# Optimization experiments

Measured on AMD Instinct MI355X. Metric: run time of the kernel, lower is better.

The kernel has to match this reference:

```python
import jax, jax.numpy as jnp
import numpy as np

BS, LATENT, HID, MAXLEN = 128, 512, 1024, 512

def setup_inputs() -> dict:
    key = jax.random.key(0)
    ks = jax.random.split(key, 12)
    s = 1.0 / np.sqrt(HID)  # pytorch default LSTM init scale
    inp = {}
    inp["decoder_input"] = jax.random.normal(ks[0], (BS, LATENT), jnp.float32)
    inp["lengths"] = jax.random.randint(ks[1], (BS,), 0, MAXLEN)
    # bidirectional single-layer LSTM params (gate order i,f,g,o; combined bias = b_ih+b_hh)
    inp["Wih_f"] = jax.random.uniform(ks[2], (4 * HID, LATENT), jnp.float32, -s, s)
    inp["Whh_f"] = jax.random.uniform(ks[3], (4 * HID, HID), jnp.float32, -s, s)
    inp["b_f"] = jax.random.uniform(ks[4], (4 * HID,), jnp.float32, -s, s)
    inp["Wih_b"] = jax.random.uniform(ks[5], (4 * HID, LATENT), jnp.float32, -s, s)
    inp["Whh_b"] = jax.random.uniform(ks[6], (4 * HID, HID), jnp.float32, -s, s)
    inp["b_b"] = jax.random.uniform(ks[7], (4 * HID,), jnp.float32, -s, s)
    # out: Linear(hidden -> latent); fc1: Linear(2*hidden -> 1)
    inp["W_out"] = jax.random.uniform(ks[8], (LATENT, HID), jnp.float32, -s, s)
    inp["b_out"] = jax.random.uniform(ks[9], (LATENT,), jnp.float32, -s, s)
    inp["W_fc1"] = jax.random.uniform(ks[10], (1, 2 * HID), jnp.float32, -s, s)
    inp["b_fc1"] = jax.random.uniform(ks[11], (1,), jnp.float32, -s, s)
    return inp

def _lstm_cell(x, h, c, Wih, Whh, b):
    z = x @ Wih.T + h @ Whh.T + b  # (bs, 4H)
    i, f, g, o = jnp.split(z, 4, axis=-1)
    c2 = jax.nn.sigmoid(f) * c + jax.nn.sigmoid(i) * jnp.tanh(g)
    h2 = jax.nn.sigmoid(o) * jnp.tanh(c2)
    return h2, c2

def reference(decoder_input, lengths, Wih_f, Whh_f, b_f, Wih_b, Whh_b, b_b,
              W_out, b_out, W_fc1, b_fc1):
    max_len = int(jnp.max(lengths))  # static decode length
    bs = decoder_input.shape[0]
    h0 = jnp.zeros((bs, HID), decoder_input.dtype)

    def step(carry, _):
        x, hf, cf, hb, cb = carry
        # bidirectional LSTM over a length-1 sequence = two cells on same input
        hf, cf = _lstm_cell(x, hf, cf, Wih_f, Whh_f, b_f)
        hb, cb = _lstm_cell(x, hb, cb, Wih_b, Whh_b, b_b)
        out_t = jnp.concatenate([hf, hb], axis=-1)  # (bs, 2H)
        # next input = out(h_n[-1]) i.e. backward-direction hidden
        x_next = hb @ W_out.T + b_out
        return (x_next, hf, cf, hb, cb), out_t

    carry0 = (decoder_input, h0, h0, h0, h0)
    _, outs = jax.lax.scan(step, carry0, xs=None, length=max_len)  # (T, bs, 2H)
    x = jnp.transpose(outs, (1, 0, 2))  # (bs, T, 2H)
    x = jax.nn.relu(x)
    return x @ W_fc1.T + b_fc1  # (bs, T, 1)
```

## Files before the change

kernel.cpp:

```cpp
#include <hip/hip_runtime.h>
#include <math.h>

typedef unsigned short u16;
typedef __attribute__((ext_vector_type(8))) short short8;
typedef __attribute__((ext_vector_type(4))) float f32x4;

__device__ __forceinline__ float sigm(float x) { return 1.0f / (1.0f + expf(-x)); }

__device__ __forceinline__ u16 f2bf(float x) {
    union { float f; unsigned u; } v; v.f = x;
    unsigned r = v.u + 0x7fffu + ((v.u >> 16) & 1u);
    return (u16)(r >> 16);
}
__device__ __forceinline__ float bf2f(u16 h) {
    union { unsigned u; float f; } v; v.u = ((unsigned)h) << 16;
    return v.f;
}
__device__ __forceinline__ f32x4 mfma16(short8 a, short8 b, f32x4 c) {
    return __builtin_amdgcn_mfma_f32_16x16x32_bf16(a, b, c, 0, 0, 0);
}
__device__ __forceinline__ void gl_lds16(const void* g, void* l) {
    __builtin_amdgcn_global_load_lds(
        (const __attribute__((address_space(1))) unsigned int*)g,
        (__attribute__((address_space(3))) unsigned int*)l, 16, 0, 0);
}
__device__ __forceinline__ int swz(int c) { return (c ^ (c >> 2)) & 3; }

#define FENCE() asm volatile("" ::: "memory")

#define STAGE_W(kk, buf)                                                      \
    do {                                                                      \
        gl_lds16(Wsrc + sA + (kk), sm + (buf) * 8192 + lds0);                 \
        gl_lds16(Wsrc + sB + (kk), sm + (buf) * 8192 + lds1);                 \
    } while (0)

#define LOAD_A(kk, AH_, AL_)                                                  \
    do {                                                                      \
        _Pragma("unroll") for (int ks_ = 0; ks_ < 2; ++ks_) {                 \
            AH_[ks_] = *(const short8*)(Ah + aoff + (kk) + ks_ * 32);         \
            AL_[ks_] = *(const short8*)(Al + aoff + (kk) + ks_ * 32);         \
        }                                                                     \
    } while (0)

#define COMPUTE(bix, AH_, AL_, cix)                                           \
    do {                                                                      \
        const char* bb_ = sm + (bix) * 8192;                                  \
        _Pragma("unroll") for (int ks_ = 0; ks_ < 2; ++ks_) {                 \
            short8 bh_[2], bl_[2];                                            \
            _Pragma("unroll") for (int nt_ = 0; nt_ < 2; ++nt_) {             \
                const int col_ = nt_ * 16 + l15;                              \
                const int off_ = ks_ * 2048 + col_ * 64 + ((quad ^ swz(col_)) * 16); \
                bh_[nt_] = *(const short8*)(bb_ + off_);                      \
                bl_[nt_] = *(const short8*)(bb_ + 4096 + off_);               \
            }                                                                 \
            _Pragma("unroll") for (int nt_ = 0; nt_ < 2; ++nt_) {             \
                acc[nt_] = mfma16(AH_[ks_], bh_[nt_], acc[nt_]);              \
                acc[nt_] = mfma16(AL_[ks_], bh_[nt_], acc[nt_]);              \
                acc[nt_] = mfma16(AH_[ks_], bl_[nt_], acc[nt_]);              \
            }                                                                 \
        }                                                                     \
        if (fc1w) {                                                           \
            const int kb_ = (cix) * 64 + quad * 8;                            \
            _Pragma("unroll") for (int ks_ = 0; ks_ < 2; ++ks_) {             \
                const float* wp_ = smWf + kb_ + ks_ * 32;                     \
                const f32x4 w0_ = *(const f32x4*)(wp_);                       \
                const f32x4 w1_ = *(const f32x4*)(wp_ + 4);                   \
                const short8 hv_ = AH_[ks_];                                  \
                const short8 lv_ = AL_[ks_];                                  \
                _Pragma("unroll") for (int e_ = 0; e_ < 8; ++e_) {            \
                    const float v_ = bf2f((u16)hv_[e_]) + bf2f((u16)lv_[e_]); \
                    const float wv_ = (e_ < 4) ? w0_[e_] : w1_[e_ - 4];       \
                    fsum = fmaf(fmaxf(v_, 0.0f), wv_, fsum);                  \
                }                                                             \
            }                                                                 \
        }                                                                     \
    } while (0)

#define ITER(cc, BC, BS, AHU, ALU, AHL, ALL)                                  \
    do {                                                                      \
        asm volatile("s_waitcnt vmcnt(16)" ::: "memory");                     \
        __builtin_amdgcn_s_barrier();                                         \
        FENCE();                                                              \
        STAGE_W(((cc) + 3) * 64, BS);                                         \
        FENCE();                                                              \
        LOAD_A(((cc) + 3) * 64, AHL, ALL);                                    \
        COMPUTE(BC, AHU, ALU, (cc));                                          \
    } while (0)

__global__ __launch_bounds__(256, 2) void k_step(
    const u16* __restrict__ Ah, const u16* __restrict__ Al,
    u16* __restrict__ NAh, u16* __restrict__ NAl,
    const u16* __restrict__ WH, const u16* __restrict__ WL, int wstride,
    int koff_f, int nch_f, int koff_b, int nch_b,
    const float* __restrict__ BR, float* __restrict__ CF, float* __restrict__ CB,
    const float* __restrict__ Wfc1, const float* __restrict__ bfc1,
    float* __restrict__ out, int T, int t)
{
    __shared__ __align__(16) char sm[32768];
    __shared__ __align__(16) char ze[9216];
    __shared__ __align__(16) float smWf[2048];

    const int tid = threadIdx.x, bid = blockIdx.x;
    const int w = tid >> 6, lane = tid & 63, l15 = lane & 15, quad = lane >> 4;
    const int dir = bid & 1;
    const int rest = bid >> 1;
    const int rowhalf = rest >> 7, colgrp = rest & 127;
    const int nbase = dir * 4096 + colgrp * 32;
    const int koff = dir ? koff_b : koff_f;
    const int nch  = dir ? nch_b : nch_f;
    const int r0 = rowhalf * 64 + w * 16;

    const bool fc1b = (dir == 0) && (colgrp == 0);
    const bool fc1w = fc1b && (t > 0);

    const int sp = w >> 1, skh = w & 1;
    const u16* Wsrc = sp ? WL : WH;
    size_t sA, sB;
    int lds0, lds1;
    {
        const int colA = 0 * 16 + (lane >> 2);
        const int colB = 1 * 16 + (lane >> 2);
        const int sa = (lane & 3) ^ swz(colA);
        const int sb = (lane & 3) ^ swz(colB);
        sA = (size_t)(nbase + colA) * wstride + (size_t)(koff + skh * 32 + sa * 8);
        sB = (size_t)(nbase + colB) * wstride + (size_t)(koff + skh * 32 + sb * 8);
        lds0 = sp * 4096 + skh * 2048;
        lds1 = lds0 + 1024;
    }

    const size_t aoff = (size_t)(r0 + l15) * 2048 + (size_t)(koff + quad * 8);

    f32x4 acc[2] = {};
    short8 ah0[2], al0[2], ah1[2], al1[2];
    short8 ah2[2], al2[2], ah3[2], al3[2];
    float fsum = 0.0f;

    if (fc1b) {
        const f32x4 w0 = *(const f32x4*)(Wfc1 + tid * 8);
        const f32x4 w1 = *(const f32x4*)(Wfc1 + tid * 8 + 4);
        *(f32x4*)(smWf + tid * 8) = w0;
        *(f32x4*)(smWf + tid * 8 + 4) = w1;
    }
    asm volatile("s_waitcnt lgkmcnt(0)" ::: "memory");

    STAGE_W(0, 0);   FENCE(); LOAD_A(0, ah0, al0);   FENCE();
    STAGE_W(64, 1);  FENCE(); LOAD_A(64, ah1, al1);  FENCE();
    STAGE_W(128, 2); FENCE(); LOAD_A(128, ah2, al2); FENCE();

    for (int c = 0; c < nch; c += 4) {
        ITER(c + 0, 0, 3, ah0, al0, ah3, al3);
        ITER(c + 1, 1, 0, ah1, al1, ah0, al0);
        ITER(c + 2, 2, 1, ah2, al2, ah1, al1);
        ITER(c + 3, 3, 2, ah3, al3, ah2, al2);
    }
    asm volatile("s_waitcnt vmcnt(0)" ::: "memory");

    if (fc1w) {
        float v = fsum;
        v += __shfl_xor(v, 16);
        v += __shfl_xor(v, 32);
        if (lane < 16)
            out[(size_t)(r0 + l15) * T + (t - 1)] = v + bfc1[0];
    }

    char* zb = ze + w * 2304;
#pragma unroll
    for (int nt = 0; nt < 2; ++nt)
#pragma unroll
        for (int r = 0; r < 4; ++r)
            *(float*)(zb + (quad * 4 + r) * 144 + (nt * 16 + l15) * 4) = acc[nt][r];

    float* C = dir ? CB : CF;
    const int ul = lane & 7;
#pragma unroll
    for (int p2 = 0; p2 < 2; ++p2) {
        const int ml = p2 * 8 + (lane >> 3);
        const f32x4 z = *(const f32x4*)(zb + ml * 144 + ul * 16);
        const f32x4 b4 = *(const f32x4*)(BR + nbase + ul * 4);
        const float zi = z[0] + b4[0], zf = z[1] + b4[1];
        const float zg = z[2] + b4[2], zo = z[3] + b4[3];
        const int u = colgrp * 8 + ul;
        const int m = r0 + ml;
        const size_t cidx = (size_t)m * 1024 + u;
        const float cold = C[cidx];
        const float c2 = sigm(zf) * cold + sigm(zi) * tanhf(zg);
        const float h2 = sigm(zo) * tanhf(c2);
        C[cidx] = c2;
        const size_t hidx = (size_t)m * 2048 + dir * 1024 + u;
        const u16 hh = f2bf(h2);
        NAh[hidx] = hh;
        NAl[hidx] = f2bf(h2 - bf2f(hh));
    }
}

__global__ __launch_bounds__(256) void k_tail(
    const u16* __restrict__ Ah, const u16* __restrict__ Al,
    const float* __restrict__ Wfc1, const float* __restrict__ bfc1,
    float* __restrict__ out, int T)
{
    __shared__ float red[256];
    const int m = blockIdx.x, tid = threadIdx.x;
    const size_t base = (size_t)m * 2048 + tid * 8;
    const short8 hv = *(const short8*)(Ah + base);
    const short8 lv = *(const short8*)(Al + base);
    float s = 0.0f;
#pragma unroll
    for (int e = 0; e < 8; ++e) {
        const float v = bf2f((u16)hv[e]) + bf2f((u16)lv[e]);
        s = fmaf(fmaxf(v, 0.0f), Wfc1[tid * 8 + e], s);
    }
    red[tid] = s;
    __syncthreads();
    for (int off = 128; off > 0; off >>= 1) {
        if (tid < off) red[tid] += red[tid + off];
        __syncthreads();
    }
    if (tid == 0) out[(size_t)m * T + T - 1] = red[0] + bfc1[0];
}

__global__ __launch_bounds__(256, 1) void k_fold(
    const u16* __restrict__ AH, const u16* __restrict__ AL,
    const u16* __restrict__ BH, const u16* __restrict__ BL,
    const float* __restrict__ Whh_b,
    u16* __restrict__ WH, u16* __restrict__ WL)
{
    const int tid = threadIdx.x, bid = blockIdx.x;
    const int w = tid >> 6, lane = tid & 63, l15 = lane & 15, quad = lane >> 4;
    const int bm = bid >> 4, bn = bid & 15;
    const int ar0 = bm * 64 + (w & 1) * 32;
    const int br0 = bn * 64 + (w >> 1) * 32;
    f32x4 acc[2][2] = {};
    for (int k0 = 0; k0 < 512; k0 += 32) {
        short8 a_h[2], a_l[2], b_h[2], b_l[2];
#pragma unroll
        for (int mt = 0; mt < 2; ++mt) {
            const size_t o = (size_t)(ar0 + mt * 16 + l15) * 512 + k0 + quad * 8;
            a_h[mt] = *(const short8*)(AH + o);
            a_l[mt] = *(const short8*)(AL + o);
        }
#pragma unroll
        for (int nt = 0; nt < 2; ++nt) {
            const size_t o = (size_t)(br0 + nt * 16 + l15) * 512 + k0 + quad * 8;
            b_h[nt] = *(const short8*)(BH + o);
            b_l[nt] = *(const short8*)(BL + o);
        }
#pragma unroll
        for (int mt = 0; mt < 2; ++mt)
#pragma unroll
            for (int nt = 0; nt < 2; ++nt) {
                acc[mt][nt] = mfma16(a_h[mt], b_h[nt], acc[mt][nt]);
                acc[mt][nt] = mfma16(a_l[mt], b_h[nt], acc[mt][nt]);
                acc[mt][nt] = mfma16(a_h[mt], b_l[nt], acc[mt][nt]);
            }
    }
#pragma unroll
    for (int mt = 0; mt < 2; ++mt)
#pragma unroll
        for (int nt = 0; nt < 2; ++nt)
#pragma unroll
            for (int r = 0; r < 4; ++r) {
                const int row = ar0 + mt * 16 + quad * 4 + r;
                const int j = br0 + nt * 16 + l15;
                float v = acc[mt][nt][r];
                if (row >= 4096)
                    v += Whh_b[(size_t)((row & 3) * 1024 + ((row & 4095) >> 2)) * 1024 + j];
                const size_t d = (size_t)row * 2048 + 1024 + j;
                const u16 hh = f2bf(v);
                WH[d] = hh;
                WL[d] = f2bf(v - bf2f(hh));
            }
}

__global__ __launch_bounds__(256) void k_prep(
    const float* __restrict__ dec,
    const float* __restrict__ Wih_f, const float* __restrict__ Whh_f,
    const float* __restrict__ b_f, const float* __restrict__ Wih_b,
    const float* __restrict__ b_b, const float* __restrict__ W_out,
    const float* __restrict__ b_out, const float* __restrict__ b_fc1,
    u16* __restrict__ WihH, u16* __restrict__ WihL,
    u16* __restrict__ WoTH, u16* __restrict__ WoTL,
    float* __restrict__ BR0, float* __restrict__ BR1,
    u16* __restrict__ A0h, u16* __restrict__ A0l,
    u16* __restrict__ WH, u16* __restrict__ WL,
    float* __restrict__ out, int out_size)
{
    const int t = blockIdx.x * 256 + threadIdx.x;
    if (t < 524288) {
        const int colp = t >> 6, kb = (t & 63) * 8;
        const int dir = colp >> 12, u = (colp & 4095) >> 2, g = colp & 3;
        const float* src = (dir ? Wih_b : Wih_f) + (size_t)(g * 1024 + u) * 512 + kb;
        const size_t d = (size_t)colp * 512 + kb;
#pragma unroll
        for (int j = 0; j < 8; ++j) {
            const float v = src[j];
            const u16 hh = f2bf(v);
            WihH[d + j] = hh; WihL[d + j] = f2bf(v - bf2f(hh));
        }
    } else if (t < 589824) {
        const int i = t - 524288, jc = i >> 6, lb = (i & 63) * 8;
#pragma unroll
        for (int jj = 0; jj < 8; ++jj) {
            const float v = W_out[(size_t)(lb + jj) * 1024 + jc];
            const size_t d = (size_t)jc * 512 + lb + jj;
            const u16 hh = f2bf(v);
            WoTH[d] = hh; WoTL[d] = f2bf(v - bf2f(hh));
        }
    } else if (t < 598016) {
        const int colp = t - 589824;
        const int dir = colp >> 12, u = (colp & 4095) >> 2, g = colp & 3;
        const float* Wih = dir ? Wih_b : Wih_f;
        const float s = (dir ? b_b : b_f)[g * 1024 + u];
        BR0[colp] = s;
        float dot = 0.0f;
        for (int l = 0; l < 512; ++l)
            dot += Wih[(size_t)(g * 1024 + u) * 512 + l] * b_out[l];
        BR1[colp] = s + dot;
    } else if (t < 606208) {
        const int i = t - 598016, m = i >> 6, kb = (i & 63) * 8;
#pragma unroll
        for (int j = 0; j < 8; ++j) {
            const float v = dec[(size_t)m * 512 + kb + j];
            const size_t d = (size_t)m * 2048 + kb + j;
            const u16 hh = f2bf(v);
            A0h[d] = hh; A0l[d] = f2bf(v - bf2f(hh));
        }
    } else if (t < 614400) {
        const int base = (t - 606208) * 8;
        const float b0 = b_fc1[0];
#pragma unroll
        for (int j = 0; j < 8; ++j)
            if (base + j < out_size) out[base + j] = b0;
    } else {
        const int i = t - 614400, colp = i >> 7, kb = (i & 127) * 8;
        const int u = colp >> 2, g = colp & 3;
        const float* src = Whh_f + (size_t)(g * 1024 + u) * 1024 + kb;
        const size_t d = (size_t)colp * 2048 + kb;
#pragma unroll
        for (int j = 0; j < 8; ++j) {
            const float v = src[j];
            const u16 hh = f2bf(v);
            WH[d + j] = hh; WL[d + j] = f2bf(v - bf2f(hh));
        }
    }
}

extern "C" void kernel_launch(void* const* d_in, const int* in_sizes, int n_in,
                              void* d_out, int out_size, void* d_ws, size_t ws_size,
                              hipStream_t stream) {
    const float* dec   = (const float*)d_in[0];
    const float* Wih_f = (const float*)d_in[2];
    const float* Whh_f = (const float*)d_in[3];
    const float* b_f   = (const float*)d_in[4];
    const float* Wih_b = (const float*)d_in[5];
    const float* Whh_b = (const float*)d_in[6];
    const float* b_b   = (const float*)d_in[7];
    const float* W_out = (const float*)d_in[8];
    const float* b_out = (const float*)d_in[9];
    const float* W_fc1 = (const float*)d_in[10];
    const float* b_fc1 = (const float*)d_in[11];
    float* out = (float*)d_out;

    char* ws = (char*)d_ws;
    u16* WH    = (u16*)(ws);
    u16* WL    = (u16*)(ws + 33554432);
    u16* WihH  = (u16*)(ws + 67108864);
    u16* WihL  = (u16*)(ws + 75497472);
    u16* WoTH  = (u16*)(ws + 83886080);
    u16* WoTL  = (u16*)(ws + 84934656);
    u16* A0h   = (u16*)(ws + 85983232);
    u16* A0l   = (u16*)(ws + 86507520);
    u16* A1h   = (u16*)(ws + 87031808);
    u16* A1l   = (u16*)(ws + 87556096);
    float* CF  = (float*)(ws + 88080384);
    float* CB  = (float*)(ws + 88604672);
    float* BR0 = (float*)(ws + 89128960);
    float* BR1 = (float*)(ws + 89161728);

    k_prep<<<4448, 256, 0, stream>>>(dec, Wih_f, Whh_f, b_f, Wih_b, b_b,
                                     W_out, b_out, b_fc1,
                                     WihH, WihL, WoTH, WoTL, BR0, BR1,
                                     A0h, A0l, WH, WL, out, out_size);
    k_fold<<<2048, 256, 0, stream>>>(WihH, WihL, WoTH, WoTL, Whh_b, WH, WL);
    hipMemsetAsync(CF, 0, 1048576, stream);

    const int T = out_size / 128;
    u16* Abh[2] = {A0h, A1h};
    u16* Abl[2] = {A0l, A1l};
    for (int t = 0; t < T; ++t) {
        const int in = t & 1, nx = in ^ 1;
        if (t == 0) {
            k_step<<<512, 256, 0, stream>>>(A0h, A0l, A1h, A1l,
                                            WihH, WihL, 512, 0, 8, 0, 8,
                                            BR0, CF, CB, W_fc1, b_fc1, out, T, 0);
        } else {
            k_step<<<512, 256, 0, stream>>>(Abh[in], Abl[in], Abh[nx], Abl[nx],
                                            WH, WL, 2048, 0, 32, 1024, 16,
                                            BR1, CF, CB, W_fc1, b_fc1, out, T, t);
        }
    }
    k_tail<<<128, 256, 0, stream>>>(Abh[T & 1], Abl[T & 1], W_fc1, b_fc1, out, T);
}
```

Baseline: 20.79 ms.

## Merge row halves into 512-thread blocks sharing staged weight tiles

Each block now covers all 128 batch rows with 8 waves instead of two 256-thread blocks each covering 64 rows, so every weight column tile is staged into LDS once per block rather than twice. Each wave issues one global-to-LDS copy per chunk instead of two, and the vmcnt wait threshold is adjusted to match. The grid halves to 256 blocks, which can lower CU coverage on a large GPU and raises LDS per block (larger epilogue buffer), possibly limiting occupancy.

```diff
diff --git a/kernel.cpp b/kernel.cpp
--- a/kernel.cpp
+++ b/kernel.cpp
@@ -29,10 +29,7 @@
 #define FENCE() asm volatile("" ::: "memory")
 
 #define STAGE_W(kk, buf)                                                      \
-    do {                                                                      \
-        gl_lds16(Wsrc + sA + (kk), sm + (buf) * 8192 + lds0);                 \
-        gl_lds16(Wsrc + sB + (kk), sm + (buf) * 8192 + lds1);                 \
-    } while (0)
+    gl_lds16(Wsrc + sA + (kk), sm + (buf) * 8192 + lds0)
 
 #define LOAD_A(kk, AH_, AL_)                                                  \
     do {                                                                      \
@@ -78,7 +75,7 @@
 
 #define ITER(cc, BC, BS, AHU, ALU, AHL, ALL)                                  \
     do {                                                                      \
-        asm volatile("s_waitcnt vmcnt(16)" ::: "memory");                     \
+        asm volatile("s_waitcnt vmcnt(14)" ::: "memory");                     \
         __builtin_amdgcn_s_barrier();                                         \
         FENCE();                                                              \
         STAGE_W(((cc) + 3) * 64, BS);                                         \
@@ -87,7 +84,7 @@
         COMPUTE(BC, AHU, ALU, (cc));                                          \
     } while (0)
 
-__global__ __launch_bounds__(256, 2) void k_step(
+__global__ __launch_bounds__(512, 2) void k_step(
     const u16* __restrict__ Ah, const u16* __restrict__ Al,
     u16* __restrict__ NAh, u16* __restrict__ NAl,
     const u16* __restrict__ WH, const u16* __restrict__ WL, int wstride,
@@ -97,35 +94,30 @@
     float* __restrict__ out, int T, int t)
 {
     __shared__ __align__(16) char sm[32768];
-    __shared__ __align__(16) char ze[9216];
+    __shared__ __align__(16) char ze[18432];
     __shared__ __align__(16) float smWf[2048];
 
     const int tid = threadIdx.x, bid = blockIdx.x;
     const int w = tid >> 6, lane = tid & 63, l15 = lane & 15, quad = lane >> 4;
     const int dir = bid & 1;
-    const int rest = bid >> 1;
-    const int rowhalf = rest >> 7, colgrp = rest & 127;
+    const int colgrp = bid >> 1;
     const int nbase = dir * 4096 + colgrp * 32;
     const int koff = dir ? koff_b : koff_f;
     const int nch  = dir ? nch_b : nch_f;
-    const int r0 = rowhalf * 64 + w * 16;
+    const int r0 = w * 16;
 
     const bool fc1b = (dir == 0) && (colgrp == 0);
     const bool fc1w = fc1b && (t > 0);
 
-    const int sp = w >> 1, skh = w & 1;
+    const int sp = w >> 2, skh = (w >> 1) & 1, ci = w & 1;
     const u16* Wsrc = sp ? WL : WH;
-    size_t sA, sB;
-    int lds0, lds1;
+    size_t sA;
+    int lds0;
     {
-        const int colA = 0 * 16 + (lane >> 2);
-        const int colB = 1 * 16 + (lane >> 2);
-        const int sa = (lane & 3) ^ swz(colA);
-        const int sb = (lane & 3) ^ swz(colB);
-        sA = (size_t)(nbase + colA) * wstride + (size_t)(koff + skh * 32 + sa * 8);
-        sB = (size_t)(nbase + colB) * wstride + (size_t)(koff + skh * 32 + sb * 8);
-        lds0 = sp * 4096 + skh * 2048;
-        lds1 = lds0 + 1024;
+        const int col = ci * 16 + (lane >> 2);
+        const int s = (lane & 3) ^ swz(col);
+        sA = (size_t)(nbase + col) * wstride + (size_t)(koff + skh * 32 + s * 8);
+        lds0 = sp * 4096 + skh * 2048 + ci * 1024;
     }
 
     const size_t aoff = (size_t)(r0 + l15) * 2048 + (size_t)(koff + quad * 8);
@@ -135,13 +127,13 @@
     short8 ah2[2], al2[2], ah3[2], al3[2];
     float fsum = 0.0f;
 
-    if (fc1b) {
+    if (fc1b && tid < 256) {
         const f32x4 w0 = *(const f32x4*)(Wfc1 + tid * 8);
         const f32x4 w1 = *(const f32x4*)(Wfc1 + tid * 8 + 4);
         *(f32x4*)(smWf + tid * 8) = w0;
         *(f32x4*)(smWf + tid * 8 + 4) = w1;
     }
-    asm volatile("s_waitcnt lgkmcnt(0)" ::: "memory");
+    asm volatile("s_waitcnt vmcnt(0) lgkmcnt(0)" ::: "memory");
 
     STAGE_W(0, 0);   FENCE(); LOAD_A(0, ah0, al0);   FENCE();
     STAGE_W(64, 1);  FENCE(); LOAD_A(64, ah1, al1);  FENCE();
@@ -389,11 +381,11 @@
     for (int t = 0; t < T; ++t) {
         const int in = t & 1, nx = in ^ 1;
         if (t == 0) {
-            k_step<<<512, 256, 0, stream>>>(A0h, A0l, A1h, A1l,
+            k_step<<<256, 512, 0, stream>>>(A0h, A0l, A1h, A1l,
                                             WihH, WihL, 512, 0, 8, 0, 8,
                                             BR0, CF, CB, W_fc1, b_fc1, out, T, 0);
         } else {
-            k_step<<<512, 256, 0, stream>>>(Abh[in], Abl[in], Abh[nx], Abl[nx],
+            k_step<<<256, 512, 0, stream>>>(Abh[in], Abl[in], Abh[nx], Abl[nx],
                                             WH, WL, 2048, 0, 32, 1024, 16,
                                             BR1, CF, CB, W_fc1, b_fc1, out, T, t);
         }
```

Result: slower. 21.64 ms (+4.1%).
